# Performance work log

Measured on AMD Instinct MI355X. Metric: run time of the kernel, lower is better.

The kernel has to match this reference:

```python
import jax, jax.numpy as jnp
import numpy as np

B, N, DEG = 128, 512, 8          # graphs, nodes per graph, avg degree
E = B * N * DEG                  # 524288 edges
F_IN, H1, H2, C = 128, 64, 128, 10
RATIO = 0.8
K = int(np.ceil(RATIO * N))      # TopKPooling keeps ceil(0.8*N)=410 nodes per graph


def setup_inputs() -> dict:
    key = jax.random.key(0)
    ks = jax.random.split(key, 10)
    n_nodes = B * N
    x = jax.random.normal(ks[0], (n_nodes, F_IN), dtype=jnp.float32)
    # random intra-graph edges, then offset node ids per graph
    src = jax.random.randint(ks[1], (B, N * DEG), 0, N)
    dst = jax.random.randint(ks[2], (B, N * DEG), 0, N)
    off = (jnp.arange(B) * N)[:, None]
    edge_index = jnp.stack([(src + off).reshape(-1), (dst + off).reshape(-1)]).astype(jnp.int64)
    batch = jnp.repeat(jnp.arange(B), N).astype(jnp.int64)
    s1 = 1.0 / np.sqrt(F_IN)
    s2 = 1.0 / np.sqrt(H1)
    s3 = 1.0 / np.sqrt(H2)
    return {
        "x": x,
        "edge_index": edge_index,
        "batch": batch,
        "W1": jax.random.uniform(ks[3], (F_IN, H1), jnp.float32, -s1, s1),
        "b1": jnp.zeros((H1,), jnp.float32),
        "W2": jax.random.uniform(ks[4], (H1, H2), jnp.float32, -s2, s2),
        "b2": jnp.zeros((H2,), jnp.float32),
        "pool_w": jax.random.uniform(ks[5], (H2,), jnp.float32, -s3, s3),
        "fc_W": jax.random.uniform(ks[6], (H2, C), jnp.float32, -s3, s3),
        "fc_b": jax.random.uniform(ks[7], (C,), jnp.float32, -s3, s3),
    }


def gcn_conv(x, W, b, src, dst, num_nodes):
    # PyG GCNConv: add self-loops, symmetric normalization, scatter-add aggregation
    loop = jnp.arange(num_nodes)
    src = jnp.concatenate([src, loop])
    dst = jnp.concatenate([dst, loop])
    deg = jax.ops.segment_sum(jnp.ones_like(src, dtype=x.dtype), dst, num_segments=num_nodes)
    dis = jnp.where(deg > 0, jax.lax.rsqrt(jnp.maximum(deg, 1.0)), 0.0)
    norm = dis[src] * dis[dst]                       # [E+N]
    h = x @ W                                        # transform first (smaller of the two in conv1)
    out = jax.ops.segment_sum(norm[:, None] * h[src], dst, num_segments=num_nodes)
    return out + b


def reference(x, edge_index, batch, W1, b1, W2, b2, pool_w, fc_W, fc_b):
    num_nodes = x.shape[0]
    src, dst = edge_index[0], edge_index[1]
    x = jax.nn.relu(gcn_conv(x, W1, b1, src, dst, num_nodes))
    x = jax.nn.relu(gcn_conv(x, W2, b2, src, dst, num_nodes))
    # TopKPooling: score = (x . w)/||w||, per-graph top-k on raw score, gate by tanh(score)
    score = (x @ pool_w) / jnp.linalg.norm(pool_w)   # [B*N]
    score_b = score.reshape(B, N)
    top_vals, top_idx = jax.lax.top_k(score_b, K)    # [B, K]
    x_b = x.reshape(B, N, H2)
    x_sel = jnp.take_along_axis(x_b, top_idx[:, :, None], axis=1)   # [B, K, H2]
    x_sel = x_sel * jnp.tanh(top_vals)[:, :, None]
    # global max pool over each (pooled) graph; pooled edge_index is unused downstream
    g = jnp.max(x_sel, axis=1)                        # [B, H2]
    logits = g @ fc_W + fc_b                          # [B, C]
    return jax.nn.log_softmax(logits, axis=1)
```

## Files before the change

kernel.cpp:

```cpp
#include <hip/hip_runtime.h>
#include <hip/hip_bf16.h>


#define BB 128
#define NN 512
#define NODES (BB*NN)
#define EE (BB*NN*8)
#define EDGPG (NN*8)
#define F_IN 128
#define H1 64
#define H2 128
#define NC 10
#define KSEL 410
#define EPG (NN*8 + NN)
#define TOT_ADJ (EE + NODES)

typedef unsigned short u16;
typedef unsigned int   u32;

static __device__ __forceinline__ float lo2f(u32 u){ return __uint_as_float(u << 16); }
static __device__ __forceinline__ float hi2f(u32 u){ return __uint_as_float(u & 0xffff0000u); }
static __device__ __forceinline__ u16 f2b(float f){
    __hip_bfloat16 h = __float2bfloat16(f);
    return *reinterpret_cast<u16*>(&h);
}
static __device__ __forceinline__ u32 packbf(float a, float b){
    return (u32)f2b(a) | ((u32)f2b(b) << 16);
}

static __device__ __forceinline__ bool ei_is_i64(const int* __restrict__ ei){
    return ((ei[1] | ei[3] | ei[5] | ei[7]) == 0);
}
static __device__ __forceinline__ int ld_src(const int* __restrict__ ei, int e, bool w64){
    return w64 ? ei[2*e] : ei[e];
}
static __device__ __forceinline__ int ld_dst(const int* __restrict__ ei, int e, bool w64){
    return w64 ? ei[2*(EE + e)] : ei[EE + e];
}

__global__ __launch_bounds__(512) void k_build(const int* __restrict__ ei,
                                               int* __restrict__ row_start,
                                               int* __restrict__ cnt_g,
                                               float* __restrict__ dis,
                                               int* __restrict__ adj){
    __shared__ int cnt[NN];
    __shared__ int sh[NN];
    __shared__ int cur[NN];
    bool w64 = ei_is_i64(ei);
    int b = blockIdx.x, t = threadIdx.x;
    cnt[t] = 0;
    __syncthreads();
    int e0 = b*EDGPG;
    for (int i = t; i < EDGPG; i += 512){
        int d = (ld_dst(ei, e0 + i, w64) - b*NN) & (NN - 1);
        atomicAdd(&cnt[d], 1);
    }
    __syncthreads();
    int tot = cnt[t] + 1;
    sh[t] = tot;
    __syncthreads();
    for (int off = 1; off < NN; off <<= 1){
        int v = (t >= off) ? sh[t-off] : 0;
        __syncthreads();
        sh[t] += v;
        __syncthreads();
    }
    int rs_local = sh[t] - tot;
    row_start[b*NN + t] = b*EPG + rs_local;
    cnt_g[b*NN + t]     = tot - 1;
    dis[b*NN + t]       = rsqrtf((float)tot);
    cur[t] = rs_local;
    __syncthreads();
    {
        int p = atomicAdd(&cur[t], 1);
        adj[b*EPG + p] = b*NN + t;
    }
    for (int i = t; i < EDGPG; i += 512){
        int d = (ld_dst(ei, e0 + i, w64) - b*NN) & (NN - 1);
        int s = ld_src(ei, e0 + i, w64) & (NODES - 1);
        int p = atomicAdd(&cur[d], 1);
        adj[b*EPG + p] = s;
    }
}

#define G1NODES 64
#define XPAD 68
__global__ __launch_bounds__(256) void k_gemm1(const float* __restrict__ x,
                                               const float* __restrict__ W1,
                                               const float* __restrict__ dis,
                                               u32* __restrict__ h1u){
    __shared__ __align__(16) float Ws[64*H1];
    __shared__ __align__(16) float xs[G1NODES*XPAD];
    int t = threadIdx.x;
    int node0 = blockIdx.x*G1NODES;
    int tc = t & 15, tr = t >> 4;
    int j0 = tc*4, n0 = tr*4;
    float acc[4][4] = {};
    for (int half = 0; half < 2; ++half){
        const float4* Wv = (const float4*)(W1 + half*4096);
        for (int i = t; i < 1024; i += 256)
            *(float4*)&Ws[i*4] = Wv[i];
        for (int i = t; i < 1024; i += 256){
            int node = i >> 4, c = i & 15;
            float4 v = *(const float4*)(x + (size_t)(node0 + node)*F_IN + half*64 + c*4);
            *(float4*)&xs[node*XPAD + c*4] = v;
        }
        __syncthreads();
        #pragma unroll 4
        for (int k = 0; k < 64; ++k){
            float4 wv = *(const float4*)&Ws[k*H1 + j0];
            float x0 = xs[(n0+0)*XPAD + k];
            float x1 = xs[(n0+1)*XPAD + k];
            float x2 = xs[(n0+2)*XPAD + k];
            float x3 = xs[(n0+3)*XPAD + k];
            acc[0][0] += x0*wv.x; acc[0][1] += x0*wv.y; acc[0][2] += x0*wv.z; acc[0][3] += x0*wv.w;
            acc[1][0] += x1*wv.x; acc[1][1] += x1*wv.y; acc[1][2] += x1*wv.z; acc[1][3] += x1*wv.w;
            acc[2][0] += x2*wv.x; acc[2][1] += x2*wv.y; acc[2][2] += x2*wv.z; acc[2][3] += x2*wv.w;
            acc[3][0] += x3*wv.x; acc[3][1] += x3*wv.y; acc[3][2] += x3*wv.z; acc[3][3] += x3*wv.w;
        }
        __syncthreads();
    }
    #pragma unroll
    for (int i = 0; i < 4; ++i){
        float dn = dis[node0 + n0 + i];
        size_t base = (size_t)(node0 + n0 + i)*32 + tc*2;
        h1u[base]     = packbf(dn*acc[i][0], dn*acc[i][1]);
        h1u[base + 1] = packbf(dn*acc[i][2], dn*acc[i][3]);
    }
}

__global__ __launch_bounds__(256) void k_agg1(const u32* __restrict__ h1u,
                                              const int* __restrict__ row_start,
                                              const int* __restrict__ cnt,
                                              const int* __restrict__ adj,
                                              const float* __restrict__ dis,
                                              const float* __restrict__ b1,
                                              u32* __restrict__ a1u){
    int t = threadIdx.x;
    int node = blockIdx.x*8 + (t >> 5);
    int fl = t & 31;
    int rs = row_start[node];
    int deg = cnt[node] + 1; if (deg > EPG) deg = EPG;
    int pe = rs + deg;
    float l0=0.f,h0=0.f,l1=0.f,h1_=0.f,l2=0.f,h2=0.f,l3=0.f,h3=0.f;
    int p = rs;
    for (; p + 4 <= pe; p += 4){
        int s0 = adj[p], s1 = adj[p+1], s2 = adj[p+2], s3 = adj[p+3];
        u32 v0 = h1u[s0*32 + fl];
        u32 v1 = h1u[s1*32 + fl];
        u32 v2 = h1u[s2*32 + fl];
        u32 v3 = h1u[s3*32 + fl];
        l0 += lo2f(v0); h0 += hi2f(v0);
        l1 += lo2f(v1); h1_ += hi2f(v1);
        l2 += lo2f(v2); h2 += hi2f(v2);
        l3 += lo2f(v3); h3 += hi2f(v3);
    }
    for (; p < pe; ++p){
        int s = adj[p]; u32 v = h1u[s*32 + fl];
        l0 += lo2f(v); h0 += hi2f(v);
    }
    float al = (l0+l1)+(l2+l3), ah = (h0+h1_)+(h2+h3);
    float dn = dis[node];
    float vl = dn*al + b1[2*fl];     vl = vl > 0.f ? vl : 0.f;
    float vh = dn*ah + b1[2*fl + 1]; vh = vh > 0.f ? vh : 0.f;
    a1u[node*32 + fl] = packbf(dn*vl, dn*vh);
}

__global__ __launch_bounds__(256) void k_aggpre(const u32* __restrict__ a1u,
                                                const int* __restrict__ row_start,
                                                const int* __restrict__ cnt,
                                                const int* __restrict__ adj,
                                                const float* __restrict__ dis,
                                                u32* __restrict__ aggu){
    int t = threadIdx.x;
    int node = blockIdx.x*8 + (t >> 5);
    int fl = t & 31;
    int rs = row_start[node];
    int deg = cnt[node] + 1; if (deg > EPG) deg = EPG;
    int pe = rs + deg;
    float l0=0.f,h0=0.f,l1=0.f,h1_=0.f,l2=0.f,h2=0.f,l3=0.f,h3=0.f;
    int p = rs;
    for (; p + 4 <= pe; p += 4){
        int s0 = adj[p], s1 = adj[p+1], s2 = adj[p+2], s3 = adj[p+3];
        u32 v0 = a1u[s0*32 + fl];
        u32 v1 = a1u[s1*32 + fl];
        u32 v2 = a1u[s2*32 + fl];
        u32 v3 = a1u[s3*32 + fl];
        l0 += lo2f(v0); h0 += hi2f(v0);
        l1 += lo2f(v1); h1_ += hi2f(v1);
        l2 += lo2f(v2); h2 += hi2f(v2);
        l3 += lo2f(v3); h3 += hi2f(v3);
    }
    for (; p < pe; ++p){
        int s = adj[p]; u32 v = a1u[s*32 + fl];
        l0 += lo2f(v); h0 += hi2f(v);
    }
    float al = (l0+l1)+(l2+l3), ah = (h0+h1_)+(h2+h3);
    float dn = dis[node];
    aggu[node*32 + fl] = packbf(dn*al, dn*ah);
}

#define G2NODES 32
#define APAD 68
__global__ __launch_bounds__(256) void k_gemm2s(const u32* __restrict__ aggu,
                                                const float* __restrict__ W2,
                                                const float* __restrict__ b2,
                                                const float* __restrict__ pw,
                                                u32* __restrict__ a2u,
                                                float* __restrict__ score){
    __shared__ __align__(16) float Ws[32*H2];
    __shared__ __align__(16) float as[G2NODES*APAD];
    __shared__ float pws[H2];
    int t = threadIdx.x;
    int node0 = blockIdx.x*G2NODES;
    int tc = t & 31, tr = t >> 5;
    int j0 = tc*4, n0 = tr*4;
    if (t < H2) pws[t] = pw[t];
    for (int i = t; i < 1024; i += 256){
        int node = i >> 5, kw = i & 31;
        u32 v = aggu[(node0 + node)*32 + kw];
        float* d = &as[node*APAD + 2*kw];
        d[0] = lo2f(v); d[1] = hi2f(v);
    }
    float acc[4][4] = {};
    for (int half = 0; half < 2; ++half){
        const float4* Wv = (const float4*)(W2 + half*4096);
        for (int i = t; i < 1024; i += 256)
            *(float4*)&Ws[i*4] = Wv[i];
        __syncthreads();
        int kb = half*32;
        #pragma unroll 4
        for (int k = 0; k < 32; ++k){
            float4 wv = *(const float4*)&Ws[k*H2 + j0];
            float x0 = as[(n0+0)*APAD + kb + k];
            float x1 = as[(n0+1)*APAD + kb + k];
            float x2 = as[(n0+2)*APAD + kb + k];
            float x3 = as[(n0+3)*APAD + kb + k];
            acc[0][0] += x0*wv.x; acc[0][1] += x0*wv.y; acc[0][2] += x0*wv.z; acc[0][3] += x0*wv.w;
            acc[1][0] += x1*wv.x; acc[1][1] += x1*wv.y; acc[1][2] += x1*wv.z; acc[1][3] += x1*wv.w;
            acc[2][0] += x2*wv.x; acc[2][1] += x2*wv.y; acc[2][2] += x2*wv.z; acc[2][3] += x2*wv.w;
            acc[3][0] += x3*wv.x; acc[3][1] += x3*wv.y; acc[3][2] += x3*wv.z; acc[3][3] += x3*wv.w;
        }
        __syncthreads();
    }
    float p0 = pws[j0], p1 = pws[j0+1], p2 = pws[j0+2], p3 = pws[j0+3];
    float bj0 = b2[j0], bj1 = b2[j0+1], bj2 = b2[j0+2], bj3 = b2[j0+3];
    #pragma unroll
    for (int i = 0; i < 4; ++i){
        float v0 = acc[i][0] + bj0; v0 = v0 > 0.f ? v0 : 0.f;
        float v1 = acc[i][1] + bj1; v1 = v1 > 0.f ? v1 : 0.f;
        float v2 = acc[i][2] + bj2; v2 = v2 > 0.f ? v2 : 0.f;
        float v3 = acc[i][3] + bj3; v3 = v3 > 0.f ? v3 : 0.f;
        size_t base = (size_t)(node0 + n0 + i)*64 + tc*2;
        a2u[base]     = packbf(v0, v1);
        a2u[base + 1] = packbf(v2, v3);
        float sp = v0*p0 + v1*p1 + v2*p2 + v3*p3;
        sp += __shfl_xor(sp, 16, 32);
        sp += __shfl_xor(sp,  8, 32);
        sp += __shfl_xor(sp,  4, 32);
        sp += __shfl_xor(sp,  2, 32);
        sp += __shfl_xor(sp,  1, 32);
        if (tc == 0) score[node0 + n0 + i] = sp;
    }
}

__global__ __launch_bounds__(512) void k_pool(const u32* __restrict__ a2u,
                                              const float* __restrict__ score,
                                              const float* __restrict__ pw,
                                              const float* __restrict__ fcW,
                                              const float* __restrict__ fcb,
                                              float* __restrict__ out){
    __shared__ float so[NN];
    __shared__ float ss[NN];
    __shared__ float th[NN];
    __shared__ float pm[16*H2];
    __shared__ float gl[H2];
    __shared__ float fws[H2*NC];
    __shared__ float lg[NC];
    __shared__ float red[3];
    int b = blockIdx.x, t = threadIdx.x;
    for (int i = t; i < H2*NC; i += 512) fws[i] = fcW[i];
    if (t < H2){ float v = pw[t]; gl[t] = v*v; }
    __syncthreads();
    if (t == 0){
        float s = 0.f;
        for (int i = 0; i < H2; ++i) s += gl[i];
        red[2] = rsqrtf(s);
    }
    __syncthreads();
    float pwinv = red[2];
    float sc = score[b*NN + t];
    so[t] = sc; ss[t] = sc; th[t] = tanhf(sc*pwinv);
    __syncthreads();
    for (int k = 2; k <= NN; k <<= 1){
        for (int j = k >> 1; j > 0; j >>= 1){
            int ixj = t ^ j;
            if (ixj > t){
                float a = ss[t], c = ss[ixj];
                bool desc = ((t & k) == 0);
                bool sw = desc ? (a < c) : (a > c);
                if (sw){ ss[t] = c; ss[ixj] = a; }
            }
            __syncthreads();
        }
    }
    float thresh = ss[KSEL-1];
    float mask_t = (so[t] >= thresh) ? 0.f : -INFINITY;
    __syncthreads();
    so[t] = mask_t;
    __syncthreads();
    int tc = t & 31, q = t >> 5;
    const uint2* ap = (const uint2*)(a2u + (size_t)b*NN*64);
    float m0 = -INFINITY, m1 = -INFINITY, m2 = -INFINITY, m3 = -INFINITY;
    int nb = q*32;
    #pragma unroll 4
    for (int n = nb; n < nb + 32; ++n){
        uint2 v = ap[(size_t)n*32 + tc];
        float thn = th[n], son = so[n];
        m0 = fmaxf(m0, lo2f(v.x)*thn + son);
        m1 = fmaxf(m1, hi2f(v.x)*thn + son);
        m2 = fmaxf(m2, lo2f(v.y)*thn + son);
        m3 = fmaxf(m3, hi2f(v.y)*thn + son);
    }
    pm[q*H2 + 4*tc]     = m0;
    pm[q*H2 + 4*tc + 1] = m1;
    pm[q*H2 + 4*tc + 2] = m2;
    pm[q*H2 + 4*tc + 3] = m3;
    __syncthreads();
    if (t < H2){
        float g = pm[t];
        #pragma unroll
        for (int qq = 1; qq < 16; ++qq) g = fmaxf(g, pm[qq*H2 + t]);
        gl[t] = g;
    }
    __syncthreads();
    if (t < NC){
        float acc = fcb[t];
        for (int k2 = 0; k2 < H2; ++k2) acc += gl[k2]*fws[k2*NC + t];
        lg[t] = acc;
    }
    __syncthreads();
    if (t == 0){
        float mx = lg[0];
        for (int i = 1; i < NC; ++i) mx = fmaxf(mx, lg[i]);
        float s = 0.f;
        for (int i = 0; i < NC; ++i) s += expf(lg[i] - mx);
        red[0] = mx; red[1] = logf(s);
    }
    __syncthreads();
    if (t < NC) out[b*NC + t] = lg[t] - red[0] - red[1];
}

extern "C" void kernel_launch(void* const* d_in, const int* in_sizes, int n_in,
                              void* d_out, int out_size, void* d_ws, size_t ws_size,
                              hipStream_t stream) {
    const float* x   = (const float*)d_in[0];
    const int*   ei  = (const int*)d_in[1];
    const float* W1  = (const float*)d_in[3];
    const float* b1  = (const float*)d_in[4];
    const float* W2  = (const float*)d_in[5];
    const float* b2  = (const float*)d_in[6];
    const float* pw  = (const float*)d_in[7];
    const float* fcW = (const float*)d_in[8];
    const float* fcb = (const float*)d_in[9];

    char* ws = (char*)d_ws;
    int*   cnt       = (int*)(ws + 4096);
    int*   row_start = (int*)(ws + 266240);
    float* dis       = (float*)(ws + 528384);
    float* score     = (float*)(ws + 790528);
    int*   adj       = (int*)(ws + 1052672);
    u32*   h1u       = (u32*)(ws + 4194304);
    u32*   a1u       = (u32*)(ws + 12582912);
    u32*   aggu      = (u32*)(ws + 4194304);
    u32*   a2u       = (u32*)(ws + 12582912);

    k_build<<<BB, 512, 0, stream>>>(ei, row_start, cnt, dis, adj);
    k_gemm1<<<NODES/G1NODES, 256, 0, stream>>>(x, W1, dis, h1u);
    k_agg1<<<NODES/8, 256, 0, stream>>>(h1u, row_start, cnt, adj, dis, b1, a1u);
    k_aggpre<<<NODES/8, 256, 0, stream>>>(a1u, row_start, cnt, adj, dis, aggu);
    k_gemm2s<<<NODES/G2NODES, 256, 0, stream>>>(aggu, W2, b2, pw, a2u, score);
    k_pool<<<BB, 512, 0, stream>>>(a2u, score, pw, fcW, fcb, (float*)d_out);
}
```

Before: 192.6 us.

## Fuse second-layer aggregation into GEMM2 and widen gather loads to uint2

The separate k_aggpre kernel is removed. Its neighbour aggregation of layer-1 activations now runs inside k_gemm2s, writing aggregated rows straight into shared memory, which removes one launch and a global round-trip of the intermediate. Both aggregation paths now use 16 lanes per node with 8-byte uint2 loads (four bf16 features per lane) instead of 32 lanes with 4-byte loads. The a2u buffer moves to a new workspace offset so it no longer aliases a1u, which the fused kernel still reads.

```diff
diff --git a/kernel.cpp b/kernel.cpp
--- a/kernel.cpp
+++ b/kernel.cpp
@@ -129,80 +129,57 @@
     }
 }
 
-__global__ __launch_bounds__(256) void k_agg1(const u32* __restrict__ h1u,
+__global__ __launch_bounds__(256) void k_agg1(const uint2* __restrict__ h1v,
                                               const int* __restrict__ row_start,
                                               const int* __restrict__ cnt,
                                               const int* __restrict__ adj,
                                               const float* __restrict__ dis,
-                                              const float* __restrict__ b1,
-                                              u32* __restrict__ a1u){
+                                              const float4* __restrict__ b1v,
+                                              uint2* __restrict__ a1v){
     int t = threadIdx.x;
-    int node = blockIdx.x*8 + (t >> 5);
-    int fl = t & 31;
+    int node = blockIdx.x*16 + (t >> 4);
+    int fl = t & 15;
     int rs = row_start[node];
     int deg = cnt[node] + 1; if (deg > EPG) deg = EPG;
     int pe = rs + deg;
-    float l0=0.f,h0=0.f,l1=0.f,h1_=0.f,l2=0.f,h2=0.f,l3=0.f,h3=0.f;
+    float a0[4] = {}, a1r[4] = {}, a2r[4] = {}, a3r[4] = {};
     int p = rs;
     for (; p + 4 <= pe; p += 4){
         int s0 = adj[p], s1 = adj[p+1], s2 = adj[p+2], s3 = adj[p+3];
-        u32 v0 = h1u[s0*32 + fl];
-        u32 v1 = h1u[s1*32 + fl];
-        u32 v2 = h1u[s2*32 + fl];
-        u32 v3 = h1u[s3*32 + fl];
-        l0 += lo2f(v0); h0 += hi2f(v0);
-        l1 += lo2f(v1); h1_ += hi2f(v1);
-        l2 += lo2f(v2); h2 += hi2f(v2);
-        l3 += lo2f(v3); h3 += hi2f(v3);
+        uint2 v0 = h1v[s0*16 + fl];
+        uint2 v1 = h1v[s1*16 + fl];
+        uint2 v2 = h1v[s2*16 + fl];
+        uint2 v3 = h1v[s3*16 + fl];
+        a0[0] += lo2f(v0.x); a0[1] += hi2f(v0.x); a0[2] += lo2f(v0.y); a0[3] += hi2f(v0.y);
+        a1r[0] += lo2f(v1.x); a1r[1] += hi2f(v1.x); a1r[2] += lo2f(v1.y); a1r[3] += hi2f(v1.y);
+        a2r[0] += lo2f(v2.x); a2r[1] += hi2f(v2.x); a2r[2] += lo2f(v2.y); a2r[3] += hi2f(v2.y);
+        a3r[0] += lo2f(v3.x); a3r[1] += hi2f(v3.x); a3r[2] += lo2f(v3.y); a3r[3] += hi2f(v3.y);
     }
     for (; p < pe; ++p){
-        int s = adj[p]; u32 v = h1u[s*32 + fl];
-        l0 += lo2f(v); h0 += hi2f(v);
-    }
-    float al = (l0+l1)+(l2+l3), ah = (h0+h1_)+(h2+h3);
+        int s = adj[p];
+        uint2 v = h1v[s*16 + fl];
+        a0[0] += lo2f(v.x); a0[1] += hi2f(v.x); a0[2] += lo2f(v.y); a0[3] += hi2f(v.y);
+    }
+    float r0 = (a0[0] + a1r[0]) + (a2r[0] + a3r[0]);
+    float r1 = (a0[1] + a1r[1]) + (a2r[1] + a3r[1]);
+    float r2 = (a0[2] + a1r[2]) + (a2r[2] + a3r[2]);
+    float r3 = (a0[3] + a1r[3]) + (a2r[3] + a3r[3]);
     float dn = dis[node];
-    float vl = dn*al + b1[2*fl];     vl = vl > 0.f ? vl : 0.f;
-    float vh = dn*ah + b1[2*fl + 1]; vh = vh > 0.f ? vh : 0.f;
-    a1u[node*32 + fl] = packbf(dn*vl, dn*vh);
-}
-
-__global__ __launch_bounds__(256) void k_aggpre(const u32* __restrict__ a1u,
+    float4 bb = b1v[fl];
+    float w0 = dn*r0 + bb.x; w0 = w0 > 0.f ? w0 : 0.f;
+    float w1 = dn*r1 + bb.y; w1 = w1 > 0.f ? w1 : 0.f;
+    float w2 = dn*r2 + bb.z; w2 = w2 > 0.f ? w2 : 0.f;
+    float w3 = dn*r3 + bb.w; w3 = w3 > 0.f ? w3 : 0.f;
+    a1v[node*16 + fl] = make_uint2(packbf(dn*w0, dn*w1), packbf(dn*w2, dn*w3));
+}
+
+#define G2NODES 32
+#define APAD 68
+__global__ __launch_bounds__(256) void k_gemm2s(const uint2* __restrict__ a1v,
                                                 const int* __restrict__ row_start,
                                                 const int* __restrict__ cnt,
                                                 const int* __restrict__ adj,
                                                 const float* __restrict__ dis,
-                                                u32* __restrict__ aggu){
-    int t = threadIdx.x;
-    int node = blockIdx.x*8 + (t >> 5);
-    int fl = t & 31;
-    int rs = row_start[node];
-    int deg = cnt[node] + 1; if (deg > EPG) deg = EPG;
-    int pe = rs + deg;
-    float l0=0.f,h0=0.f,l1=0.f,h1_=0.f,l2=0.f,h2=0.f,l3=0.f,h3=0.f;
-    int p = rs;
-    for (; p + 4 <= pe; p += 4){
-        int s0 = adj[p], s1 = adj[p+1], s2 = adj[p+2], s3 = adj[p+3];
-        u32 v0 = a1u[s0*32 + fl];
-        u32 v1 = a1u[s1*32 + fl];
-        u32 v2 = a1u[s2*32 + fl];
-        u32 v3 = a1u[s3*32 + fl];
-        l0 += lo2f(v0); h0 += hi2f(v0);
-        l1 += lo2f(v1); h1_ += hi2f(v1);
-        l2 += lo2f(v2); h2 += hi2f(v2);
-        l3 += lo2f(v3); h3 += hi2f(v3);
-    }
-    for (; p < pe; ++p){
-        int s = adj[p]; u32 v = a1u[s*32 + fl];
-        l0 += lo2f(v); h0 += hi2f(v);
-    }
-    float al = (l0+l1)+(l2+l3), ah = (h0+h1_)+(h2+h3);
-    float dn = dis[node];
-    aggu[node*32 + fl] = packbf(dn*al, dn*ah);
-}
-
-#define G2NODES 32
-#define APAD 68
-__global__ __launch_bounds__(256) void k_gemm2s(const u32* __restrict__ aggu,
                                                 const float* __restrict__ W2,
                                                 const float* __restrict__ b2,
                                                 const float* __restrict__ pw,
@@ -213,15 +190,43 @@
     __shared__ float pws[H2];
     int t = threadIdx.x;
     int node0 = blockIdx.x*G2NODES;
+    if (t < H2) pws[t] = pw[t];
+    {
+        int fl = t & 15, ng = t >> 4;
+        for (int pass = 0; pass < 2; ++pass){
+            int nl = ng + pass*16;
+            int node = node0 + nl;
+            int rs = row_start[node];
+            int deg = cnt[node] + 1; if (deg > EPG) deg = EPG;
+            int pe = rs + deg;
+            float a0[4] = {}, a1r[4] = {}, a2r[4] = {}, a3r[4] = {};
+            int p = rs;
+            for (; p + 4 <= pe; p += 4){
+                int s0 = adj[p], s1 = adj[p+1], s2 = adj[p+2], s3 = adj[p+3];
+                uint2 v0 = a1v[s0*16 + fl];
+                uint2 v1 = a1v[s1*16 + fl];
+                uint2 v2 = a1v[s2*16 + fl];
+                uint2 v3 = a1v[s3*16 + fl];
+                a0[0] += lo2f(v0.x); a0[1] += hi2f(v0.x); a0[2] += lo2f(v0.y); a0[3] += hi2f(v0.y);
+                a1r[0] += lo2f(v1.x); a1r[1] += hi2f(v1.x); a1r[2] += lo2f(v1.y); a1r[3] += hi2f(v1.y);
+                a2r[0] += lo2f(v2.x); a2r[1] += hi2f(v2.x); a2r[2] += lo2f(v2.y); a2r[3] += hi2f(v2.y);
+                a3r[0] += lo2f(v3.x); a3r[1] += hi2f(v3.x); a3r[2] += lo2f(v3.y); a3r[3] += hi2f(v3.y);
+            }
+            for (; p < pe; ++p){
+                int s = adj[p];
+                uint2 v = a1v[s*16 + fl];
+                a0[0] += lo2f(v.x); a0[1] += hi2f(v.x); a0[2] += lo2f(v.y); a0[3] += hi2f(v.y);
+            }
+            float dn = dis[node];
+            float* dst = &as[nl*APAD + 4*fl];
+            dst[0] = dn*((a0[0] + a1r[0]) + (a2r[0] + a3r[0]));
+            dst[1] = dn*((a0[1] + a1r[1]) + (a2r[1] + a3r[1]));
+            dst[2] = dn*((a0[2] + a1r[2]) + (a2r[2] + a3r[2]));
+            dst[3] = dn*((a0[3] + a1r[3]) + (a2r[3] + a3r[3]));
+        }
+    }
     int tc = t & 31, tr = t >> 5;
     int j0 = tc*4, n0 = tr*4;
-    if (t < H2) pws[t] = pw[t];
-    for (int i = t; i < 1024; i += 256){
-        int node = i >> 5, kw = i & 31;
-        u32 v = aggu[(node0 + node)*32 + kw];
-        float* d = &as[node*APAD + 2*kw];
-        d[0] = lo2f(v); d[1] = hi2f(v);
-    }
     float acc[4][4] = {};
     for (int half = 0; half < 2; ++half){
         const float4* Wv = (const float4*)(W2 + half*4096);
@@ -372,13 +377,13 @@
     int*   adj       = (int*)(ws + 1052672);
     u32*   h1u       = (u32*)(ws + 4194304);
     u32*   a1u       = (u32*)(ws + 12582912);
-    u32*   aggu      = (u32*)(ws + 4194304);
-    u32*   a2u       = (u32*)(ws + 12582912);
+    u32*   a2u       = (u32*)(ws + 20971520);
 
     k_build<<<BB, 512, 0, stream>>>(ei, row_start, cnt, dis, adj);
     k_gemm1<<<NODES/G1NODES, 256, 0, stream>>>(x, W1, dis, h1u);
-    k_agg1<<<NODES/8, 256, 0, stream>>>(h1u, row_start, cnt, adj, dis, b1, a1u);
-    k_aggpre<<<NODES/8, 256, 0, stream>>>(a1u, row_start, cnt, adj, dis, aggu);
-    k_gemm2s<<<NODES/G2NODES, 256, 0, stream>>>(aggu, W2, b2, pw, a2u, score);
+    k_agg1<<<NODES/16, 256, 0, stream>>>((const uint2*)h1u, row_start, cnt, adj, dis,
+                                         (const float4*)b1, (uint2*)a1u);
+    k_gemm2s<<<NODES/G2NODES, 256, 0, stream>>>((const uint2*)a1u, row_start, cnt, adj,
+                                                dis, W2, b2, pw, a2u, score);
     k_pool<<<BB, 512, 0, stream>>>(a2u, score, pw, fcW, fcb, (float*)d_out);
 }
```

Result: faster. 177.4 us (-7.9%).
